# Kernel optimization log

Hardware: AMD Instinct MI355X
Metric: run time of the kernel (lower is better)

The kernel has to match this reference:

```python
import jax, jax.numpy as jnp
import numpy as np

V, E, L, H, C, NC = 32000, 128, 256, 2048, 256, 10   # vocab, embed, seq_len, ae_hidden, cnn_out/d_model, classes
D_INNER, D_STATE, DT_RANK, D_CONV = 512, 16, 16, 4    # mamba defaults for d_model=256 (expand=2)
B = 64


def setup_inputs() -> dict:
    key = jax.random.key(0)
    ks = jax.random.split(key, 20)
    def rn(k, shape, s=0.02):
        return jax.random.normal(k, shape, jnp.float32) * s
    return {
        "x": jax.random.randint(ks[0], (B, L), 0, V),
        "embed": rn(ks[1], (V, E), 1.0),
        "enc_w1": rn(ks[2], (H, E * L)), "enc_b1": jnp.zeros((H,), jnp.float32),
        "enc_w2": rn(ks[3], (E * L, H)), "enc_b2": jnp.zeros((E * L,), jnp.float32),
        "conv_w": rn(ks[4], (C, E, 5)), "conv_b": jnp.zeros((C,), jnp.float32),
        "in_proj_w": rn(ks[5], (2 * D_INNER, C)),
        "conv1d_w": rn(ks[6], (D_INNER, 1, D_CONV)), "conv1d_b": jnp.zeros((D_INNER,), jnp.float32),
        "x_proj_w": rn(ks[7], (DT_RANK + 2 * D_STATE, D_INNER)),
        "dt_proj_w": rn(ks[8], (D_INNER, DT_RANK), 0.1),
        "dt_proj_b": rn(ks[9], (D_INNER,), 0.1),
        "A_log": jnp.log(jnp.broadcast_to(jnp.arange(1, D_STATE + 1, dtype=jnp.float32), (D_INNER, D_STATE))),
        "D": jnp.ones((D_INNER,), jnp.float32),
        "out_proj_w": rn(ks[10], (C, D_INNER)),
        "fc_w": rn(ks[11], (NC, C)), "fc_b": jnp.zeros((NC,), jnp.float32),
    }


def _mamba(xs, in_proj_w, conv1d_w, conv1d_b, x_proj_w, dt_proj_w, dt_proj_b, A_log, Dp, out_proj_w):
    # xs: (B, Lp, C)
    xz = xs @ in_proj_w.T                                   # (B, Lp, 2*d_inner)
    u, z = jnp.split(xz, 2, axis=-1)
    # causal depthwise conv1d + SiLU
    u_c = u.transpose(0, 2, 1)                              # (B, d_inner, Lp)
    u_c = jnp.pad(u_c, ((0, 0), (0, 0), (D_CONV - 1, 0)))
    u_c = jax.lax.conv_general_dilated(
        u_c, conv1d_w, window_strides=(1,), padding=[(0, 0)],
        dimension_numbers=("NCH", "OIH", "NCH"), feature_group_count=D_INNER)
    u = jax.nn.silu((u_c + conv1d_b[None, :, None]).transpose(0, 2, 1))  # (B, Lp, d_inner)
    # input-dependent dt, B, C
    xdbl = u @ x_proj_w.T
    dt, Bm, Cm = jnp.split(xdbl, [DT_RANK, DT_RANK + D_STATE], axis=-1)
    delta = jax.nn.softplus(dt @ dt_proj_w.T + dt_proj_b)   # (B, Lp, d_inner)
    A = -jnp.exp(A_log)                                     # (d_inner, d_state)
    dA = jnp.exp(jnp.einsum("bld,dn->bldn", delta, A))      # (B, Lp, d_inner, d_state)
    dBu = (delta * u)[..., None] * Bm[:, :, None, :]        # (B, Lp, d_inner, d_state)
    # sequential selective scan over time
    def step(h, inp):
        dA_t, dBu_t, c_t = inp
        h = dA_t * h + dBu_t                                # (B, d_inner, d_state)
        y = jnp.einsum("bdn,bn->bd", h, c_t)
        return h, y
    h0 = jnp.zeros((xs.shape[0], D_INNER, D_STATE), xs.dtype)
    _, ys = jax.lax.scan(step, h0, (dA.transpose(1, 0, 2, 3), dBu.transpose(1, 0, 2, 3), Cm.transpose(1, 0, 2)))
    y = ys.transpose(1, 0, 2) + u * Dp                      # (B, Lp, d_inner)
    y = y * jax.nn.silu(z)
    return y @ out_proj_w.T                                 # (B, Lp, C)


def reference(x, embed, enc_w1, enc_b1, enc_w2, enc_b2, conv_w, conv_b,
              in_proj_w, conv1d_w, conv1d_b, x_proj_w, dt_proj_w, dt_proj_b,
              A_log, D, out_proj_w, fc_w, fc_b):
    b = x.shape[0]
    e = embed[x].reshape(b, -1)                             # (B, E*L)
    h = jax.nn.relu(e @ enc_w1.T + enc_b1)
    h = jax.nn.relu(h @ enc_w2.T + enc_b2)
    h = h.reshape(b, L, E).transpose(0, 2, 1)               # (B, E, L)
    h = jax.lax.conv_general_dilated(h, conv_w, window_strides=(1,), padding=[(2, 2)],
                                     dimension_numbers=("NCH", "OIH", "NCH"))
    h = jax.nn.relu(h + conv_b[None, :, None])              # (B, C, L)
    h = h.reshape(b, C, L // 2, 2).max(axis=-1)             # MaxPool1d(2)
    xs = h.transpose(0, 2, 1)                               # (B, L/2, C)
    y = _mamba(xs, in_proj_w, conv1d_w, conv1d_b, x_proj_w, dt_proj_w, dt_proj_b, A_log, D, out_proj_w)
    return y.mean(axis=1) @ fc_w.T + fc_b                   # (B, NC)
```

## Files before the change

### kernel.cpp

```cpp
#include <hip/hip_runtime.h>
#include <cstddef>
#include <cstdint>

#define B_   64
#define L_   256
#define E_   128
#define H_   2048
#define C_   256
#define LP_  128
#define DI_  512
#define DS_  16

typedef __attribute__((ext_vector_type(8))) short s16x8;
typedef __attribute__((ext_vector_type(4))) float f32x4;

__device__ __forceinline__ short f2bf(float x) {
  uint32_t u = __float_as_uint(x);
  uint32_t r = (u + 0x7FFFu + ((u >> 16) & 1u)) >> 16;
  return (short)r;
}
__device__ __forceinline__ float bf2f(short h) {
  return __uint_as_float(((uint32_t)(uint16_t)h) << 16);
}

__global__ __launch_bounds__(64) void embed_k(const int* __restrict__ x,
                                              const float* __restrict__ emb,
                                              float* __restrict__ e) {
  int bl = blockIdx.x;
  int idx = x[bl];
  const float2* src = (const float2*)(emb + (size_t)idx * E_);
  float2* dst = (float2*)(e + (size_t)bl * E_);
  dst[threadIdx.x] = src[threadIdx.x];
}

__global__ __launch_bounds__(256) void gemm_mfma_k(const float* __restrict__ A,
                                                   const float* __restrict__ W,
                                                   const float* __restrict__ bias,
                                                   float* __restrict__ Cout,
                                                   int M, int N, int K, int kChunk,
                                                   int act) {
  __shared__ __align__(16) short Ahi[64][40];
  __shared__ __align__(16) short Alo[64][40];
  __shared__ __align__(16) short Whi[64][40];
  __shared__ __align__(16) short Wlo[64][40];

  const int tid = threadIdx.x;
  const int r   = tid >> 2;
  const int seg = (tid & 3) * 8;
  const int lane = tid & 63;
  const int wv   = tid >> 6;
  const int ml   = lane & 15;
  const int quad = lane >> 4;
  const int bn = blockIdx.x * 64, bm = blockIdx.y * 64;
  const int kStart = blockIdx.z * kChunk, kEnd = kStart + kChunk;

  f32x4 acc[4];
#pragma unroll
  for (int nt = 0; nt < 4; ++nt) acc[nt] = (f32x4){0.f, 0.f, 0.f, 0.f};

  const float* Arow = A + (size_t)(bm + r) * K + seg;
  const float* Wrow = W + (size_t)(bn + r) * K + seg;

  float4 a0 = *(const float4*)(Arow + kStart);
  float4 a1 = *(const float4*)(Arow + kStart + 4);
  float4 w0 = *(const float4*)(Wrow + kStart);
  float4 w1 = *(const float4*)(Wrow + kStart + 4);

  for (int k0 = kStart; k0 < kEnd; k0 += 32) {
    float av[8] = {a0.x, a0.y, a0.z, a0.w, a1.x, a1.y, a1.z, a1.w};
    float wq[8] = {w0.x, w0.y, w0.z, w0.w, w1.x, w1.y, w1.z, w1.w};
    s16x8 ah, al, wh, wl;
#pragma unroll
    for (int j = 0; j < 8; ++j) {
      short h = f2bf(av[j]);
      ah[j] = h; al[j] = f2bf(av[j] - bf2f(h));
      short g = f2bf(wq[j]);
      wh[j] = g; wl[j] = f2bf(wq[j] - bf2f(g));
    }
    __syncthreads();
    *(s16x8*)&Ahi[r][seg] = ah;
    *(s16x8*)&Alo[r][seg] = al;
    *(s16x8*)&Whi[r][seg] = wh;
    *(s16x8*)&Wlo[r][seg] = wl;
    __syncthreads();
    if (k0 + 32 < kEnd) {
      a0 = *(const float4*)(Arow + k0 + 32);
      a1 = *(const float4*)(Arow + k0 + 36);
      w0 = *(const float4*)(Wrow + k0 + 32);
      w1 = *(const float4*)(Wrow + k0 + 36);
    }
    s16x8 fah = *(const s16x8*)&Ahi[wv * 16 + ml][quad * 8];
    s16x8 fal = *(const s16x8*)&Alo[wv * 16 + ml][quad * 8];
#pragma unroll
    for (int nt = 0; nt < 4; ++nt) {
      s16x8 fwh = *(const s16x8*)&Whi[nt * 16 + ml][quad * 8];
      s16x8 fwl = *(const s16x8*)&Wlo[nt * 16 + ml][quad * 8];
      acc[nt] = __builtin_amdgcn_mfma_f32_16x16x32_bf16(fah, fwh, acc[nt], 0, 0, 0);
      acc[nt] = __builtin_amdgcn_mfma_f32_16x16x32_bf16(fah, fwl, acc[nt], 0, 0, 0);
      acc[nt] = __builtin_amdgcn_mfma_f32_16x16x32_bf16(fal, fwh, acc[nt], 0, 0, 0);
    }
  }

  if (gridDim.z > 1) {
    float* P = Cout + (size_t)blockIdx.z * M * N;
#pragma unroll
    for (int nt = 0; nt < 4; ++nt) {
      int n = bn + nt * 16 + ml;
#pragma unroll
      for (int i = 0; i < 4; ++i) {
        int m = bm + wv * 16 + quad * 4 + i;
        P[(size_t)m * N + n] = acc[nt][i];
      }
    }
  } else {
#pragma unroll
    for (int nt = 0; nt < 4; ++nt) {
      int n = bn + nt * 16 + ml;
      float bv = bias ? bias[n] : 0.0f;
#pragma unroll
      for (int i = 0; i < 4; ++i) {
        int m = bm + wv * 16 + quad * 4 + i;
        float v = acc[nt][i] + bv;
        if (act) v = v > 0.0f ? v : 0.0f;
        Cout[(size_t)m * N + n] = v;
      }
    }
  }
}

__global__ __launch_bounds__(256) void reduce_k(const float* __restrict__ P,
                                                const float* __restrict__ bias,
                                                float* __restrict__ Out,
                                                int MN, int N, int S) {
  int i = blockIdx.x * 256 + threadIdx.x;
  if (i >= MN) return;
  float s = 0.0f;
  for (int z = 0; z < S; ++z) s += P[(size_t)z * MN + i];
  s += bias[i & (N - 1)];
  Out[i] = s > 0.0f ? s : 0.0f;
}

__global__ __launch_bounds__(256) void prep_convw_k(const float* __restrict__ cw,
                                                    float* __restrict__ wT) {
  int et = blockIdx.x;
  int c = threadIdx.x;
  wT[et * 256 + c] = cw[c * 640 + et];
}

__global__ __launch_bounds__(256) void prep_xpw_k(const float* __restrict__ w,
                                                  float* __restrict__ wp) {
  int i = blockIdx.x * 256 + threadIdx.x;
  int n = i >> 9, k = i & 511;
  wp[i] = (n < 48) ? w[n * 512 + k] : 0.0f;
}

__global__ __launch_bounds__(256) void conv_pool_k(const float* __restrict__ h2,
                                                   const float* __restrict__ wT,
                                                   const float* __restrict__ cb,
                                                   float* __restrict__ xs) {
  __shared__ float in[20][128];
  int b = blockIdx.x;
  int l0 = blockIdx.y * 16;
  for (int idx = threadIdx.x; idx < 20 * 128; idx += 256) {
    int r = idx >> 7, e = idx & 127;
    int l = l0 - 2 + r;
    in[r][e] = (l >= 0 && l < L_) ? h2[((size_t)b * L_ + l) * E_ + e] : 0.0f;
  }
  __syncthreads();
  int c = threadIdx.x;
  float acc[16];
  float bc = cb[c];
#pragma unroll
  for (int l = 0; l < 16; ++l) acc[l] = bc;
  for (int e = 0; e < 128; ++e) {
    float vin[20];
#pragma unroll
    for (int r = 0; r < 20; ++r) vin[r] = in[r][e];
#pragma unroll
    for (int t = 0; t < 5; ++t) {
      float w = wT[(e * 5 + t) * 256 + c];
#pragma unroll
      for (int l = 0; l < 16; ++l) acc[l] = fmaf(vin[l + t], w, acc[l]);
    }
  }
  int l2 = l0 >> 1;
#pragma unroll
  for (int p = 0; p < 8; ++p) {
    float v0 = acc[2 * p]     > 0.0f ? acc[2 * p]     : 0.0f;
    float v1 = acc[2 * p + 1] > 0.0f ? acc[2 * p + 1] : 0.0f;
    xs[((size_t)b * LP_ + l2 + p) * C_ + c] = v0 > v1 ? v0 : v1;
  }
}

__global__ __launch_bounds__(512) void dwconv_k(const float* __restrict__ xz,
                                               const float* __restrict__ cw,
                                               const float* __restrict__ cb,
                                               float* __restrict__ u2) {
  int m = blockIdx.x;
  int t = m & (LP_ - 1);
  int d = threadIdx.x;
  float4 w = *(const float4*)(cw + d * 4);
  const float* base = xz + (size_t)m * (2 * DI_) + d;
  float pre = cb[d];
  if (t >= 3) {
    pre = fmaf(base[-3 * 2 * DI_], w.x, pre);
    pre = fmaf(base[-2 * 2 * DI_], w.y, pre);
    pre = fmaf(base[-1 * 2 * DI_], w.z, pre);
    pre = fmaf(base[0],            w.w, pre);
  } else {
    const float wv[4] = {w.x, w.y, w.z, w.w};
    for (int j = 0; j < 4; ++j) {
      int tt = t - 3 + j;
      if (tt >= 0) pre = fmaf(base[(j - 3) * 2 * DI_], wv[j], pre);
    }
  }
  float s = pre / (1.0f + __expf(-pre));
  u2[(size_t)m * DI_ + d] = s;
}

__global__ __launch_bounds__(512) void delta_k(const float* __restrict__ xdbl,
                                               const float* __restrict__ dtw,
                                               const float* __restrict__ dtb,
                                               float* __restrict__ delta) {
  __shared__ float dt[16];
  int m = blockIdx.x;
  int d = threadIdx.x;
  if (d < 16) dt[d] = xdbl[(size_t)m * 64 + d];
  __syncthreads();
  float acc = dtb[d];
  const float* wr = dtw + d * 16;
#pragma unroll
  for (int r = 0; r < 16; ++r) acc = fmaf(dt[r], wr[r], acc);
  float sp = (acc > 0.0f ? acc : 0.0f) + log1pf(__expf(-fabsf(acc)));
  delta[(size_t)m * DI_ + d] = sp;
}

__global__ __launch_bounds__(256) void scan_k(const float* __restrict__ delta,
                                              const float* __restrict__ u2,
                                              const float* __restrict__ xz,
                                              const float* __restrict__ xdbl,
                                              const float* __restrict__ A_log,
                                              const float* __restrict__ Dp,
                                              float* __restrict__ yg) {
  int tid = threadIdx.x;
  int n = tid & 15;
  int ch = tid >> 4;
  int b = blockIdx.x >> 5;
  int d = ((blockIdx.x & 31) << 4) + ch;
  float An = -__expf(A_log[d * 16 + n]);
  float Dd = Dp[d];
  float h = 0.0f;
  const size_t mBase = (size_t)b * LP_;
  for (int t = 0; t < LP_; ++t) {
    size_t m = mBase + t;
    float dl = delta[m * DI_ + d];
    float uu = u2[m * DI_ + d];
    float Bn = xdbl[m * 64 + 16 + n];
    float Cn = xdbl[m * 64 + 32 + n];
    float dA = __expf(dl * An);
    h = fmaf(dA, h, (dl * uu) * Bn);
    float y = h * Cn;
    y += __shfl_xor(y, 1, 16);
    y += __shfl_xor(y, 2, 16);
    y += __shfl_xor(y, 4, 16);
    y += __shfl_xor(y, 8, 16);
    if (n == 0) {
      float zz = xz[m * (2 * DI_) + DI_ + d];
      float g = zz / (1.0f + __expf(-zz));
      yg[m * DI_ + d] = fmaf(uu, Dd, y) * g;
    }
  }
}

__global__ __launch_bounds__(256) void meanfc_k(const float* __restrict__ mout,
                                               const float* __restrict__ fcw,
                                               const float* __restrict__ fcb,
                                               float* __restrict__ out) {
  __shared__ float pooled[256];
  int b = blockIdx.x;
  int c = threadIdx.x;
  float s = 0.0f;
  for (int t = 0; t < LP_; ++t) s += mout[((size_t)b * LP_ + t) * C_ + c];
  pooled[c] = s * (1.0f / 128.0f);
  __syncthreads();
  if (c < 10) {
    float acc = fcb[c];
    for (int k = 0; k < 256; ++k) acc = fmaf(pooled[k], fcw[c * 256 + k], acc);
    out[b * 10 + c] = acc;
  }
}

extern "C" void kernel_launch(void* const* d_in, const int* in_sizes, int n_in,
                              void* d_out, int out_size, void* d_ws, size_t ws_size,
                              hipStream_t stream) {
  const int*   x         = (const int*)d_in[0];
  const float* embed     = (const float*)d_in[1];
  const float* enc_w1    = (const float*)d_in[2];
  const float* enc_b1    = (const float*)d_in[3];
  const float* enc_w2    = (const float*)d_in[4];
  const float* enc_b2    = (const float*)d_in[5];
  const float* conv_w    = (const float*)d_in[6];
  const float* conv_b    = (const float*)d_in[7];
  const float* in_proj_w = (const float*)d_in[8];
  const float* conv1d_w  = (const float*)d_in[9];
  const float* conv1d_b  = (const float*)d_in[10];
  const float* x_proj_w  = (const float*)d_in[11];
  const float* dt_proj_w = (const float*)d_in[12];
  const float* dt_proj_b = (const float*)d_in[13];
  const float* A_log     = (const float*)d_in[14];
  const float* Dp        = (const float*)d_in[15];
  const float* out_proj_w= (const float*)d_in[16];
  const float* fc_w      = (const float*)d_in[17];
  const float* fc_b      = (const float*)d_in[18];
  float* out = (float*)d_out;

  char* ws = (char*)d_ws;
  size_t off = 0;
  auto alloc = [&](size_t bytes) {
    char* p = ws + off;
    off += (bytes + 255) & ~(size_t)255;
    return p;
  };
  float*  e    = (float*) alloc(2097152ull * 4);
  float*  P    = (float*) alloc(2097152ull * 4);
  float*  h1   = (float*) alloc(131072ull  * 4);
  float*  h2   = (float*) alloc(2097152ull * 4);
  float*  wT   = (float*) alloc(163840ull  * 4);
  float*  xs   = (float*) alloc(2097152ull * 4);
  float*  xz   = (float*) alloc(8388608ull * 4);
  float*  u2   = (float*) alloc(4194304ull * 4);
  float*  xpw  = (float*) alloc(32768ull   * 4);
  float*  xdbl = (float*) alloc(524288ull  * 4);
  float*  dl   = (float*) alloc(4194304ull * 4);
  float*  yg   = (float*) alloc(4194304ull * 4);
  float*  mout = (float*) alloc(2097152ull * 4);
  (void)ws_size; (void)in_sizes; (void)n_in; (void)out_size;

  embed_k<<<16384, 64, 0, stream>>>(x, embed, e);
  prep_convw_k<<<640, 256, 0, stream>>>(conv_w, wT);
  prep_xpw_k<<<128, 256, 0, stream>>>(x_proj_w, xpw);

  gemm_mfma_k<<<dim3(32, 1, 16), 256, 0, stream>>>(e, enc_w1, nullptr, P,
                                                   64, 2048, 32768, 2048, 0);
  reduce_k<<<512, 256, 0, stream>>>(P, enc_b1, h1, 131072, 2048, 16);

  gemm_mfma_k<<<dim3(512, 1, 1), 256, 0, stream>>>(h1, enc_w2, enc_b2, h2,
                                                   64, 32768, 2048, 2048, 1);

  conv_pool_k<<<dim3(64, 16), 256, 0, stream>>>(h2, wT, conv_b, xs);

  gemm_mfma_k<<<dim3(16, 128, 1), 256, 0, stream>>>(xs, in_proj_w, nullptr, xz,
                                                    8192, 1024, 256, 256, 0);

  dwconv_k<<<8192, 512, 0, stream>>>(xz, conv1d_w, conv1d_b, u2);

  gemm_mfma_k<<<dim3(1, 128, 1), 256, 0, stream>>>(u2, xpw, nullptr, xdbl,
                                                   8192, 64, 512, 512, 0);

  delta_k<<<8192, 512, 0, stream>>>(xdbl, dt_proj_w, dt_proj_b, dl);

  scan_k<<<2048, 256, 0, stream>>>(dl, u2, xz, xdbl, A_log, Dp, yg);

  gemm_mfma_k<<<dim3(4, 128, 1), 256, 0, stream>>>(yg, out_proj_w, nullptr, mout,
                                                   8192, 256, 512, 512, 0);

  meanfc_k<<<64, 256, 0, stream>>>(mout, fc_w, fc_b, out);
}
```

Before: 940.0 us.

## Store activations as bf16 hi/lo pairs, fuse conv into GEMM, fuse delta into scan

The GEMM becomes a template that can read pre-split bf16 hi/lo operands, so producers emit split activations and weights are split once in a combined prep kernel. The direct conv+pool kernel is replaced by an im2col-style MFMA GEMM with a fused bias/ReLU/maxpool epilogue. The delta projection and softplus move into the scan kernel via shared memory, and the encoder split-K doubles to 32 chunks. Conversion uses the hardware packed bf16 instruction. This trades more workspace and many simultaneous changes for less conversion work and fewer kernels.

```diff
diff --git a/kernel.cpp b/kernel.cpp
--- a/kernel.cpp
+++ b/kernel.cpp
@@ -14,35 +14,92 @@
 typedef __attribute__((ext_vector_type(8))) short s16x8;
 typedef __attribute__((ext_vector_type(4))) float f32x4;
 
-__device__ __forceinline__ short f2bf(float x) {
-  uint32_t u = __float_as_uint(x);
-  uint32_t r = (u + 0x7FFFu + ((u >> 16) & 1u)) >> 16;
-  return (short)r;
-}
-__device__ __forceinline__ float bf2f(short h) {
-  return __uint_as_float(((uint32_t)(uint16_t)h) << 16);
-}
-
-__global__ __launch_bounds__(64) void embed_k(const int* __restrict__ x,
-                                              const float* __restrict__ emb,
-                                              float* __restrict__ e) {
-  int bl = blockIdx.x;
+__device__ __forceinline__ uint32_t cvt_pk_bf16(float a, float b) {
+  uint32_t r;
+  asm("v_cvt_pk_bf16_f32 %0, %1, %2" : "=v"(r) : "v"(a), "v"(b));
+  return r;
+}
+
+__device__ __forceinline__ void split1(float x, short& h, short& l) {
+  uint32_t p = cvt_pk_bf16(x, x);
+  float rres = x - __uint_as_float(p << 16);
+  uint32_t q = cvt_pk_bf16(rres, rres);
+  h = (short)p; l = (short)q;
+}
+
+__device__ __forceinline__ void cvt8(const float4& a0, const float4& a1,
+                                     s16x8& h, s16x8& l) {
+  union { uint32_t u[4]; s16x8 v; } H, L;
+  float x[8] = {a0.x, a0.y, a0.z, a0.w, a1.x, a1.y, a1.z, a1.w};
+#pragma unroll
+  for (int j = 0; j < 4; ++j) {
+    uint32_t p = cvt_pk_bf16(x[2*j], x[2*j+1]);
+    float r0 = x[2*j]   - __uint_as_float(p << 16);
+    float r1 = x[2*j+1] - __uint_as_float(p & 0xFFFF0000u);
+    H.u[j] = p;
+    L.u[j] = cvt_pk_bf16(r0, r1);
+  }
+  h = H.v; l = L.v;
+}
+
+__global__ __launch_bounds__(256) void embed_k(const int* __restrict__ x,
+                                               const float* __restrict__ emb,
+                                               short* __restrict__ ehi,
+                                               short* __restrict__ elo) {
+  int bl = blockIdx.x * 4 + (threadIdx.x >> 6);
+  int lane = threadIdx.x & 63;
   int idx = x[bl];
-  const float2* src = (const float2*)(emb + (size_t)idx * E_);
-  float2* dst = (float2*)(e + (size_t)bl * E_);
-  dst[threadIdx.x] = src[threadIdx.x];
-}
-
-__global__ __launch_bounds__(256) void gemm_mfma_k(const float* __restrict__ A,
-                                                   const float* __restrict__ W,
-                                                   const float* __restrict__ bias,
-                                                   float* __restrict__ Cout,
-                                                   int M, int N, int K, int kChunk,
-                                                   int act) {
-  __shared__ __align__(16) short Ahi[64][40];
-  __shared__ __align__(16) short Alo[64][40];
-  __shared__ __align__(16) short Whi[64][40];
-  __shared__ __align__(16) short Wlo[64][40];
+  float2 v = ((const float2*)(emb + (size_t)idx * E_))[lane];
+  uint32_t p = cvt_pk_bf16(v.x, v.y);
+  float r0 = v.x - __uint_as_float(p << 16);
+  float r1 = v.y - __uint_as_float(p & 0xFFFF0000u);
+  uint32_t q = cvt_pk_bf16(r0, r1);
+  ((uint32_t*)ehi)[(size_t)bl * 64 + lane] = p;
+  ((uint32_t*)elo)[(size_t)bl * 64 + lane] = q;
+}
+
+__global__ __launch_bounds__(256) void prep_all(
+    const float* __restrict__ conv_w, const float* __restrict__ ipw,
+    const float* __restrict__ opw,    const float* __restrict__ xpw,
+    short* __restrict__ wthi,  short* __restrict__ wtlo,
+    short* __restrict__ ipwhi, short* __restrict__ ipwlo,
+    short* __restrict__ opwhi, short* __restrict__ opwlo,
+    short* __restrict__ xpwhi, short* __restrict__ xpwlo) {
+  int blk = blockIdx.x, tid = threadIdx.x;
+  if (blk < 640) {
+    int k = blk, c = tid, t = k >> 7, e = k & 127;
+    float v = conv_w[c * 640 + e * 5 + t];
+    short h, l; split1(v, h, l);
+    wthi[(size_t)c * 640 + k] = h; wtlo[(size_t)c * 640 + k] = l;
+  } else if (blk < 640 + 1024) {
+    int n = blk - 640;
+    size_t i = (size_t)n * 256 + tid;
+    short h, l; split1(ipw[i], h, l);
+    ipwhi[i] = h; ipwlo[i] = l;
+  } else if (blk < 640 + 1024 + 512) {
+    size_t i = (size_t)(blk - 1664) * 256 + tid;
+    short h, l; split1(opw[i], h, l);
+    opwhi[i] = h; opwlo[i] = l;
+  } else {
+    int i = (blk - 2176) * 256 + tid;
+    int n = i >> 9, k = i & 511;
+    float v = (n < 48) ? xpw[n * 512 + k] : 0.0f;
+    short h, l; split1(v, h, l);
+    xpwhi[i] = h; xpwlo[i] = l;
+  }
+}
+
+template<int AM, int WM, int EPI>
+__global__ __launch_bounds__(256) void gemm_t(
+    const void* __restrict__ Aa, const void* __restrict__ Ab,
+    const void* __restrict__ Wa, const void* __restrict__ Wb,
+    const float* __restrict__ bias,
+    float* __restrict__ Cf, short* __restrict__ Chi, short* __restrict__ Clo,
+    int M, int N, int K, int kChunk) {
+  __shared__ __align__(16) short AhiS[64][40];
+  __shared__ __align__(16) short AloS[64][40];
+  __shared__ __align__(16) short WhiS[64][40];
+  __shared__ __align__(16) short WloS[64][40];
 
   const int tid = threadIdx.x;
   const int r   = tid >> 2;
@@ -58,51 +115,71 @@
 #pragma unroll
   for (int nt = 0; nt < 4; ++nt) acc[nt] = (f32x4){0.f, 0.f, 0.f, 0.f};
 
-  const float* Arow = A + (size_t)(bm + r) * K + seg;
-  const float* Wrow = W + (size_t)(bn + r) * K + seg;
-
-  float4 a0 = *(const float4*)(Arow + kStart);
-  float4 a1 = *(const float4*)(Arow + kStart + 4);
-  float4 w0 = *(const float4*)(Wrow + kStart);
-  float4 w1 = *(const float4*)(Wrow + kStart + 4);
+  auto loadA = [&](int k0, s16x8& h, s16x8& l) {
+    if constexpr (AM == 0) {
+      const float* Ar = (const float*)Aa + (size_t)(bm + r) * K + seg + k0;
+      float4 a0 = *(const float4*)Ar;
+      float4 a1 = *(const float4*)(Ar + 4);
+      cvt8(a0, a1, h, l);
+    } else if constexpr (AM == 1) {
+      size_t o = (size_t)(bm + r) * K + seg + k0;
+      h = *(const s16x8*)((const short*)Aa + o);
+      l = *(const s16x8*)((const short*)Ab + o);
+    } else {
+      int m = bm + r, bb = m >> 8, lrow = m & 255;
+      int k = k0 + seg, t = k >> 7, e = k & 127;
+      int ls = lrow + t - 2;
+      if (ls >= 0 && ls < 256) {
+        size_t o = ((size_t)bb << 15) + ((size_t)ls << 7) + (size_t)e;
+        h = *(const s16x8*)((const short*)Aa + o);
+        l = *(const s16x8*)((const short*)Ab + o);
+      } else {
+        h = (s16x8)(short)0; l = (s16x8)(short)0;
+      }
+    }
+  };
+  auto loadW = [&](int k0, s16x8& h, s16x8& l) {
+    if constexpr (WM == 0) {
+      const float* Wr = (const float*)Wa + (size_t)(bn + r) * K + seg + k0;
+      float4 w0 = *(const float4*)Wr;
+      float4 w1 = *(const float4*)(Wr + 4);
+      cvt8(w0, w1, h, l);
+    } else {
+      size_t o = (size_t)(bn + r) * K + seg + k0;
+      h = *(const s16x8*)((const short*)Wa + o);
+      l = *(const s16x8*)((const short*)Wb + o);
+    }
+  };
+
+  s16x8 pAh, pAl, pWh, pWl;
+  loadA(kStart, pAh, pAl);
+  loadW(kStart, pWh, pWl);
 
   for (int k0 = kStart; k0 < kEnd; k0 += 32) {
-    float av[8] = {a0.x, a0.y, a0.z, a0.w, a1.x, a1.y, a1.z, a1.w};
-    float wq[8] = {w0.x, w0.y, w0.z, w0.w, w1.x, w1.y, w1.z, w1.w};
-    s16x8 ah, al, wh, wl;
-#pragma unroll
-    for (int j = 0; j < 8; ++j) {
-      short h = f2bf(av[j]);
-      ah[j] = h; al[j] = f2bf(av[j] - bf2f(h));
-      short g = f2bf(wq[j]);
-      wh[j] = g; wl[j] = f2bf(wq[j] - bf2f(g));
-    }
     __syncthreads();
-    *(s16x8*)&Ahi[r][seg] = ah;
-    *(s16x8*)&Alo[r][seg] = al;
-    *(s16x8*)&Whi[r][seg] = wh;
-    *(s16x8*)&Wlo[r][seg] = wl;
+    *(s16x8*)&AhiS[r][seg] = pAh;
+    *(s16x8*)&AloS[r][seg] = pAl;
+    *(s16x8*)&WhiS[r][seg] = pWh;
+    *(s16x8*)&WloS[r][seg] = pWl;
     __syncthreads();
     if (k0 + 32 < kEnd) {
-      a0 = *(const float4*)(Arow + k0 + 32);
-      a1 = *(const float4*)(Arow + k0 + 36);
-      w0 = *(const float4*)(Wrow + k0 + 32);
-      w1 = *(const float4*)(Wrow + k0 + 36);
-    }
-    s16x8 fah = *(const s16x8*)&Ahi[wv * 16 + ml][quad * 8];
-    s16x8 fal = *(const s16x8*)&Alo[wv * 16 + ml][quad * 8];
+      loadA(k0 + 32, pAh, pAl);
+      loadW(k0 + 32, pWh, pWl);
+    }
+    s16x8 fah = *(const s16x8*)&AhiS[wv * 16 + ml][quad * 8];
+    s16x8 fal = *(const s16x8*)&AloS[wv * 16 + ml][quad * 8];
 #pragma unroll
     for (int nt = 0; nt < 4; ++nt) {
-      s16x8 fwh = *(const s16x8*)&Whi[nt * 16 + ml][quad * 8];
-      s16x8 fwl = *(const s16x8*)&Wlo[nt * 16 + ml][quad * 8];
+      s16x8 fwh = *(const s16x8*)&WhiS[nt * 16 + ml][quad * 8];
+      s16x8 fwl = *(const s16x8*)&WloS[nt * 16 + ml][quad * 8];
       acc[nt] = __builtin_amdgcn_mfma_f32_16x16x32_bf16(fah, fwh, acc[nt], 0, 0, 0);
       acc[nt] = __builtin_amdgcn_mfma_f32_16x16x32_bf16(fah, fwl, acc[nt], 0, 0, 0);
       acc[nt] = __builtin_amdgcn_mfma_f32_16x16x32_bf16(fal, fwh, acc[nt], 0, 0, 0);
     }
   }
 
-  if (gridDim.z > 1) {
-    float* P = Cout + (size_t)blockIdx.z * M * N;
+  if constexpr (EPI == 1) {
+    float* P = Cf + (size_t)blockIdx.z * ((size_t)M * N);
 #pragma unroll
     for (int nt = 0; nt < 4; ++nt) {
       int n = bn + nt * 16 + ml;
@@ -112,7 +189,7 @@
         P[(size_t)m * N + n] = acc[nt][i];
       }
     }
-  } else {
+  } else if constexpr (EPI == 0) {
 #pragma unroll
     for (int nt = 0; nt < 4; ++nt) {
       int n = bn + nt * 16 + ml;
@@ -120,82 +197,66 @@
 #pragma unroll
       for (int i = 0; i < 4; ++i) {
         int m = bm + wv * 16 + quad * 4 + i;
+        Cf[(size_t)m * N + n] = acc[nt][i] + bv;
+      }
+    }
+  } else if constexpr (EPI == 2) {
+#pragma unroll
+    for (int nt = 0; nt < 4; ++nt) {
+      int n = bn + nt * 16 + ml;
+      float bv = bias[n];
+#pragma unroll
+      for (int i = 0; i < 4; ++i) {
+        int m = bm + wv * 16 + quad * 4 + i;
         float v = acc[nt][i] + bv;
-        if (act) v = v > 0.0f ? v : 0.0f;
-        Cout[(size_t)m * N + n] = v;
+        v = v > 0.0f ? v : 0.0f;
+        short hh, ll; split1(v, hh, ll);
+        Chi[(size_t)m * N + n] = hh;
+        Clo[(size_t)m * N + n] = ll;
       }
+    }
+  } else {
+    int m0 = bm + wv * 16 + quad * 4;
+    int bb = m0 >> 8;
+    int lb = m0 & 255;
+    size_t row0 = ((size_t)bb * 128 + (lb >> 1)) * 256;
+#pragma unroll
+    for (int nt = 0; nt < 4; ++nt) {
+      int n = bn + nt * 16 + ml;
+      float bv = bias[n];
+      float v0 = fmaxf(acc[nt][0] + bv, 0.0f);
+      float v1 = fmaxf(acc[nt][1] + bv, 0.0f);
+      float v2 = fmaxf(acc[nt][2] + bv, 0.0f);
+      float v3 = fmaxf(acc[nt][3] + bv, 0.0f);
+      float p0 = fmaxf(v0, v1), p1 = fmaxf(v2, v3);
+      short hh, ll;
+      split1(p0, hh, ll);
+      Chi[row0 + n] = hh; Clo[row0 + n] = ll;
+      split1(p1, hh, ll);
+      Chi[row0 + 256 + n] = hh; Clo[row0 + 256 + n] = ll;
     }
   }
 }
 
 __global__ __launch_bounds__(256) void reduce_k(const float* __restrict__ P,
                                                 const float* __restrict__ bias,
-                                                float* __restrict__ Out,
+                                                short* __restrict__ hhi,
+                                                short* __restrict__ hlo,
                                                 int MN, int N, int S) {
   int i = blockIdx.x * 256 + threadIdx.x;
   if (i >= MN) return;
   float s = 0.0f;
   for (int z = 0; z < S; ++z) s += P[(size_t)z * MN + i];
   s += bias[i & (N - 1)];
-  Out[i] = s > 0.0f ? s : 0.0f;
-}
-
-__global__ __launch_bounds__(256) void prep_convw_k(const float* __restrict__ cw,
-                                                    float* __restrict__ wT) {
-  int et = blockIdx.x;
-  int c = threadIdx.x;
-  wT[et * 256 + c] = cw[c * 640 + et];
-}
-
-__global__ __launch_bounds__(256) void prep_xpw_k(const float* __restrict__ w,
-                                                  float* __restrict__ wp) {
-  int i = blockIdx.x * 256 + threadIdx.x;
-  int n = i >> 9, k = i & 511;
-  wp[i] = (n < 48) ? w[n * 512 + k] : 0.0f;
-}
-
-__global__ __launch_bounds__(256) void conv_pool_k(const float* __restrict__ h2,
-                                                   const float* __restrict__ wT,
-                                                   const float* __restrict__ cb,
-                                                   float* __restrict__ xs) {
-  __shared__ float in[20][128];
-  int b = blockIdx.x;
-  int l0 = blockIdx.y * 16;
-  for (int idx = threadIdx.x; idx < 20 * 128; idx += 256) {
-    int r = idx >> 7, e = idx & 127;
-    int l = l0 - 2 + r;
-    in[r][e] = (l >= 0 && l < L_) ? h2[((size_t)b * L_ + l) * E_ + e] : 0.0f;
-  }
-  __syncthreads();
-  int c = threadIdx.x;
-  float acc[16];
-  float bc = cb[c];
-#pragma unroll
-  for (int l = 0; l < 16; ++l) acc[l] = bc;
-  for (int e = 0; e < 128; ++e) {
-    float vin[20];
-#pragma unroll
-    for (int r = 0; r < 20; ++r) vin[r] = in[r][e];
-#pragma unroll
-    for (int t = 0; t < 5; ++t) {
-      float w = wT[(e * 5 + t) * 256 + c];
-#pragma unroll
-      for (int l = 0; l < 16; ++l) acc[l] = fmaf(vin[l + t], w, acc[l]);
-    }
-  }
-  int l2 = l0 >> 1;
-#pragma unroll
-  for (int p = 0; p < 8; ++p) {
-    float v0 = acc[2 * p]     > 0.0f ? acc[2 * p]     : 0.0f;
-    float v1 = acc[2 * p + 1] > 0.0f ? acc[2 * p + 1] : 0.0f;
-    xs[((size_t)b * LP_ + l2 + p) * C_ + c] = v0 > v1 ? v0 : v1;
-  }
+  s = s > 0.0f ? s : 0.0f;
+  short hh, ll; split1(s, hh, ll);
+  hhi[i] = hh; hlo[i] = ll;
 }
 
 __global__ __launch_bounds__(512) void dwconv_k(const float* __restrict__ xz,
-                                               const float* __restrict__ cw,
-                                               const float* __restrict__ cb,
-                                               float* __restrict__ u2) {
+                                                const float* __restrict__ cw,
+                                                const float* __restrict__ cb,
+                                                float* __restrict__ u2) {
   int m = blockIdx.x;
   int t = m & (LP_ - 1);
   int d = threadIdx.x;
@@ -218,42 +279,57 @@
   u2[(size_t)m * DI_ + d] = s;
 }
 
-__global__ __launch_bounds__(512) void delta_k(const float* __restrict__ xdbl,
-                                               const float* __restrict__ dtw,
-                                               const float* __restrict__ dtb,
-                                               float* __restrict__ delta) {
-  __shared__ float dt[16];
-  int m = blockIdx.x;
-  int d = threadIdx.x;
-  if (d < 16) dt[d] = xdbl[(size_t)m * 64 + d];
-  __syncthreads();
-  float acc = dtb[d];
-  const float* wr = dtw + d * 16;
-#pragma unroll
-  for (int r = 0; r < 16; ++r) acc = fmaf(dt[r], wr[r], acc);
-  float sp = (acc > 0.0f ? acc : 0.0f) + log1pf(__expf(-fabsf(acc)));
-  delta[(size_t)m * DI_ + d] = sp;
-}
-
-__global__ __launch_bounds__(256) void scan_k(const float* __restrict__ delta,
-                                              const float* __restrict__ u2,
+__global__ __launch_bounds__(256) void scan_k(const float* __restrict__ u2,
                                               const float* __restrict__ xz,
                                               const float* __restrict__ xdbl,
+                                              const float* __restrict__ dtw,
+                                              const float* __restrict__ dtb,
                                               const float* __restrict__ A_log,
                                               const float* __restrict__ Dp,
-                                              float* __restrict__ yg) {
-  int tid = threadIdx.x;
-  int n = tid & 15;
-  int ch = tid >> 4;
-  int b = blockIdx.x >> 5;
-  int d = ((blockIdx.x & 31) << 4) + ch;
+                                              short* __restrict__ yghi,
+                                              short* __restrict__ yglo) {
+  __shared__ float dls[16][128];
+  const int tid = threadIdx.x;
+  const int b = blockIdx.x >> 5;
+  const int d0 = (blockIdx.x & 31) << 4;
+  const size_t mBase = (size_t)b * LP_;
+
+  {
+    const int ch = tid >> 4;
+    const int t0 = (tid & 15) * 8;
+    const int d = d0 + ch;
+    const float4* wr = (const float4*)(dtw + d * 16);
+    float4 w0 = wr[0], w1 = wr[1], w2 = wr[2], w3 = wr[3];
+    float bdt = dtb[d];
+#pragma unroll
+    for (int j = 0; j < 8; ++j) {
+      int t = t0 + j;
+      const float4* xr = (const float4*)(xdbl + (mBase + t) * 64);
+      float4 x0 = xr[0], x1 = xr[1], x2 = xr[2], x3 = xr[3];
+      float a = bdt;
+      a = fmaf(w0.x, x0.x, a); a = fmaf(w0.y, x0.y, a);
+      a = fmaf(w0.z, x0.z, a); a = fmaf(w0.w, x0.w, a);
+      a = fmaf(w1.x, x1.x, a); a = fmaf(w1.y, x1.y, a);
+      a = fmaf(w1.z, x1.z, a); a = fmaf(w1.w, x1.w, a);
+      a = fmaf(w2.x, x2.x, a); a = fmaf(w2.y, x2.y, a);
+      a = fmaf(w2.z, x2.z, a); a = fmaf(w2.w, x2.w, a);
+      a = fmaf(w3.x, x3.x, a); a = fmaf(w3.y, x3.y, a);
+      a = fmaf(w3.z, x3.z, a); a = fmaf(w3.w, x3.w, a);
+      float sp = fmaxf(a, 0.0f) + log1pf(__expf(-fabsf(a)));
+      dls[ch][t] = sp;
+    }
+  }
+  __syncthreads();
+
+  const int n = tid & 15;
+  const int ch = tid >> 4;
+  const int d = d0 + ch;
   float An = -__expf(A_log[d * 16 + n]);
   float Dd = Dp[d];
   float h = 0.0f;
-  const size_t mBase = (size_t)b * LP_;
   for (int t = 0; t < LP_; ++t) {
     size_t m = mBase + t;
-    float dl = delta[m * DI_ + d];
+    float dl = dls[ch][t];
     float uu = u2[m * DI_ + d];
     float Bn = xdbl[m * 64 + 16 + n];
     float Cn = xdbl[m * 64 + 32 + n];
@@ -267,15 +343,18 @@
     if (n == 0) {
       float zz = xz[m * (2 * DI_) + DI_ + d];
       float g = zz / (1.0f + __expf(-zz));
-      yg[m * DI_ + d] = fmaf(uu, Dd, y) * g;
+      float yv = fmaf(uu, Dd, y) * g;
+      short hh, ll; split1(yv, hh, ll);
+      yghi[m * DI_ + d] = hh;
+      yglo[m * DI_ + d] = ll;
     }
   }
 }
 
 __global__ __launch_bounds__(256) void meanfc_k(const float* __restrict__ mout,
-                                               const float* __restrict__ fcw,
-                                               const float* __restrict__ fcb,
-                                               float* __restrict__ out) {
+                                                const float* __restrict__ fcw,
+                                                const float* __restrict__ fcb,
+                                                float* __restrict__ out) {
   __shared__ float pooled[256];
   int b = blockIdx.x;
   int c = threadIdx.x;
@@ -321,48 +400,65 @@
     off += (bytes + 255) & ~(size_t)255;
     return p;
   };
-  float*  e    = (float*) alloc(2097152ull * 4);
-  float*  P    = (float*) alloc(2097152ull * 4);
-  float*  h1   = (float*) alloc(131072ull  * 4);
-  float*  h2   = (float*) alloc(2097152ull * 4);
-  float*  wT   = (float*) alloc(163840ull  * 4);
-  float*  xs   = (float*) alloc(2097152ull * 4);
-  float*  xz   = (float*) alloc(8388608ull * 4);
-  float*  u2   = (float*) alloc(4194304ull * 4);
-  float*  xpw  = (float*) alloc(32768ull   * 4);
-  float*  xdbl = (float*) alloc(524288ull  * 4);
-  float*  dl   = (float*) alloc(4194304ull * 4);
-  float*  yg   = (float*) alloc(4194304ull * 4);
-  float*  mout = (float*) alloc(2097152ull * 4);
+  short* ehi   = (short*)alloc(2097152ull * 2);
+  short* elo   = (short*)alloc(2097152ull * 2);
+  float* P     = (float*)alloc(4194304ull * 4);
+  short* h1hi  = (short*)alloc(131072ull  * 2);
+  short* h1lo  = (short*)alloc(131072ull  * 2);
+  short* h2hi  = (short*)alloc(2097152ull * 2);
+  short* h2lo  = (short*)alloc(2097152ull * 2);
+  short* wthi  = (short*)alloc(163840ull  * 2);
+  short* wtlo  = (short*)alloc(163840ull  * 2);
+  short* ipwhi = (short*)alloc(262144ull  * 2);
+  short* ipwlo = (short*)alloc(262144ull  * 2);
+  short* xpwhi = (short*)alloc(32768ull   * 2);
+  short* xpwlo = (short*)alloc(32768ull   * 2);
+  short* opwhi = (short*)alloc(131072ull  * 2);
+  short* opwlo = (short*)alloc(131072ull  * 2);
+  short* xshi  = (short*)alloc(2097152ull * 2);
+  short* xslo  = (short*)alloc(2097152ull * 2);
+  float* xz    = (float*)alloc(8388608ull * 4);
+  float* u2    = (float*)alloc(4194304ull * 4);
+  float* xdbl  = (float*)alloc(524288ull  * 4);
+  short* yghi  = (short*)alloc(4194304ull * 2);
+  short* yglo  = (short*)alloc(4194304ull * 2);
+  float* mout  = (float*)alloc(2097152ull * 4);
   (void)ws_size; (void)in_sizes; (void)n_in; (void)out_size;
 
-  embed_k<<<16384, 64, 0, stream>>>(x, embed, e);
-  prep_convw_k<<<640, 256, 0, stream>>>(conv_w, wT);
-  prep_xpw_k<<<128, 256, 0, stream>>>(x_proj_w, xpw);
-
-  gemm_mfma_k<<<dim3(32, 1, 16), 256, 0, stream>>>(e, enc_w1, nullptr, P,
-                                                   64, 2048, 32768, 2048, 0);
-  reduce_k<<<512, 256, 0, stream>>>(P, enc_b1, h1, 131072, 2048, 16);
-
-  gemm_mfma_k<<<dim3(512, 1, 1), 256, 0, stream>>>(h1, enc_w2, enc_b2, h2,
-                                                   64, 32768, 2048, 2048, 1);
-
-  conv_pool_k<<<dim3(64, 16), 256, 0, stream>>>(h2, wT, conv_b, xs);
-
-  gemm_mfma_k<<<dim3(16, 128, 1), 256, 0, stream>>>(xs, in_proj_w, nullptr, xz,
-                                                    8192, 1024, 256, 256, 0);
+  prep_all<<<2304, 256, 0, stream>>>(conv_w, in_proj_w, out_proj_w, x_proj_w,
+                                     wthi, wtlo, ipwhi, ipwlo, opwhi, opwlo,
+                                     xpwhi, xpwlo);
+  embed_k<<<4096, 256, 0, stream>>>(x, embed, ehi, elo);
+
+  gemm_t<1, 0, 1><<<dim3(32, 1, 32), 256, 0, stream>>>(
+      ehi, elo, enc_w1, nullptr, nullptr, P, nullptr, nullptr,
+      64, 2048, 32768, 1024);
+  reduce_k<<<512, 256, 0, stream>>>(P, enc_b1, h1hi, h1lo, 131072, 2048, 32);
+
+  gemm_t<1, 0, 2><<<dim3(512, 1, 1), 256, 0, stream>>>(
+      h1hi, h1lo, enc_w2, nullptr, enc_b2, nullptr, h2hi, h2lo,
+      64, 32768, 2048, 2048);
+
+  gemm_t<2, 1, 3><<<dim3(4, 256, 1), 256, 0, stream>>>(
+      h2hi, h2lo, wthi, wtlo, conv_b, nullptr, xshi, xslo,
+      16384, 256, 640, 640);
+
+  gemm_t<1, 1, 0><<<dim3(16, 128, 1), 256, 0, stream>>>(
+      xshi, xslo, ipwhi, ipwlo, nullptr, xz, nullptr, nullptr,
+      8192, 1024, 256, 256);
 
   dwconv_k<<<8192, 512, 0, stream>>>(xz, conv1d_w, conv1d_b, u2);
 
-  gemm_mfma_k<<<dim3(1, 128, 1), 256, 0, stream>>>(u2, xpw, nullptr, xdbl,
-                                                   8192, 64, 512, 512, 0);
-
-  delta_k<<<8192, 512, 0, stream>>>(xdbl, dt_proj_w, dt_proj_b, dl);
-
-  scan_k<<<2048, 256, 0, stream>>>(dl, u2, xz, xdbl, A_log, Dp, yg);
-
-  gemm_mfma_k<<<dim3(4, 128, 1), 256, 0, stream>>>(yg, out_proj_w, nullptr, mout,
-                                                   8192, 256, 512, 512, 0);
+  gemm_t<0, 1, 0><<<dim3(1, 128, 1), 256, 0, stream>>>(
+      u2, nullptr, xpwhi, xpwlo, nullptr, xdbl, nullptr, nullptr,
+      8192, 64, 512, 512);
+
+  scan_k<<<2048, 256, 0, stream>>>(u2, xz, xdbl, dt_proj_w, dt_proj_b,
+                                   A_log, Dp, yghi, yglo);
+
+  gemm_t<1, 1, 0><<<dim3(4, 128, 1), 256, 0, stream>>>(
+      yghi, yglo, opwhi, opwlo, nullptr, mout, nullptr, nullptr,
+      8192, 256, 512, 512);
 
   meanfc_k<<<64, 256, 0, stream>>>(mout, fc_w, fc_b, out);
 }
```

Measured after the change: 963.7 us. +2.5%, slower.
